# Optimization experiments

Hardware: AMD Instinct MI355X
Metric: run time of the kernel (lower is better)

Reference implementation:

```python
import jax, jax.numpy as jnp
import numpy as np

N = 200000
F_IN = 165
H = 128
E = 3200000


def gcn_conv(x, edge_index, W, b):
    # x: [N, Fin], edge_index: [2, E], W: [Fin, Fout], b: [Fout]
    n = x.shape[0]
    h = x @ W  # linear transform first (PyG GCNConv)
    # add self loops
    loops = jnp.arange(n, dtype=edge_index.dtype)
    src = jnp.concatenate([edge_index[0], loops])
    dst = jnp.concatenate([edge_index[1], loops])
    # symmetric normalization: deg computed on dst (in-degree incl. self loops)
    deg = jax.ops.segment_sum(jnp.ones_like(dst, dtype=h.dtype), dst, num_segments=n)
    dinv = jnp.where(deg > 0, jax.lax.rsqrt(deg), 0.0)
    norm = dinv[src] * dinv[dst]  # [E+N]
    msgs = h[src] * norm[:, None]  # gather + scale
    out = jax.ops.segment_sum(msgs, dst, num_segments=n)  # scatter-add
    return out + b


def setup_inputs() -> dict:
    key = jax.random.key(0)
    k = jax.random.split(key, 8)
    x = jax.random.normal(k[0], (N, F_IN), dtype=jnp.float32)
    edge_index = jax.random.randint(k[1], (2, E), 0, N, dtype=jnp.int64)
    s1 = 1.0 / np.sqrt(F_IN)
    s2 = 1.0 / np.sqrt(H)
    W1 = jax.random.uniform(k[2], (F_IN, H), jnp.float32, -s1, s1)
    b1 = jnp.zeros((H,), jnp.float32)
    W2 = jax.random.uniform(k[3], (H, H), jnp.float32, -s2, s2)
    b2 = jnp.zeros((H,), jnp.float32)
    Wl = jax.random.uniform(k[4], (H, 2), jnp.float32, -s2, s2)
    bl = jax.random.uniform(k[5], (2,), jnp.float32, -s2, s2)
    return {"x": x, "edge_index": edge_index, "W1": W1, "b1": b1,
            "W2": W2, "b2": b2, "Wl": Wl, "bl": bl}


def reference(x, edge_index, W1, b1, W2, b2, Wl, bl):
    h = gcn_conv(x, edge_index, W1, b1)
    h = jax.nn.relu(h)
    # dropout p=0.3 is identity in eval mode
    h = gcn_conv(h, edge_index, W2, b2)
    h = jax.nn.relu(h)
    return h @ Wl + bl  # [N, 2]
```

## Files before the change

### kernel.cpp

```cpp
#include <hip/hip_runtime.h>
#include <hip/hip_bf16.h>

#define FIN 165
#define HID 128
#define NPB 256
#define MAXNB 784
#define CAP 4608
#define EPB 4096

typedef __attribute__((ext_vector_type(8))) short short8;
typedef __attribute__((ext_vector_type(4))) float float4v;

__device__ inline unsigned bf16rne(float v) {
    unsigned u = __float_as_uint(v);
    return (u + 0x7fffu + ((u >> 16) & 1u)) >> 16;
}

__device__ inline void bf16split(float v, short& h, short& l) {
    unsigned u = __float_as_uint(v);
    unsigned r = u + 0x7fffu + ((u >> 16) & 1u);
    h = (short)(r >> 16);
    float hf = __uint_as_float(((unsigned)(unsigned short)h) << 16);
    float lf = v - hf;
    unsigned u2 = __float_as_uint(lf);
    unsigned r2 = u2 + 0x7fffu + ((u2 >> 16) & 1u);
    l = (short)(r2 >> 16);
}

__global__ __launch_bounds__(256) void bucket_scatter(const int* __restrict__ src,
                                                      const int* __restrict__ dst,
                                                      int* __restrict__ gcur,
                                                      int2* __restrict__ bucketed,
                                                      int E, int n, int NB) {
    __shared__ int hist[MAXNB];
    __shared__ int base[MAXNB];
    __shared__ int lcur[MAXNB];
    int tid = threadIdx.x;
    long e0 = (long)blockIdx.x * EPB;
    for (int b = tid; b < NB; b += 256) { hist[b] = 0; lcur[b] = 0; }
    __syncthreads();
#pragma unroll
    for (int i = 0; i < EPB / 256; ++i) {
        long e = e0 + i * 256 + tid;
        if (e < E) {
            int d = dst[e], s = src[e];
            if ((unsigned)d < (unsigned)n && (unsigned)s < (unsigned)n)
                atomicAdd(&hist[d >> 8], 1);
        }
    }
    __syncthreads();
    for (int b = tid; b < NB; b += 256) {
        int h = hist[b];
        base[b] = h ? atomicAdd(&gcur[b * 16], h) : 0;
    }
    __syncthreads();
#pragma unroll
    for (int i = 0; i < EPB / 256; ++i) {
        long e = e0 + i * 256 + tid;
        if (e < E) {
            int d = dst[e], s = src[e];
            if ((unsigned)d < (unsigned)n && (unsigned)s < (unsigned)n) {
                int bk = d >> 8;
                int idx = base[bk] + atomicAdd(&lcur[bk], 1);
                if ((unsigned)idx < (unsigned)CAP)
                    bucketed[(size_t)bk * CAP + idx] = make_int2(s, d);
            }
        }
    }
}

__global__ __launch_bounds__(256) void bucket_scan(const int* __restrict__ gcur,
                                                   int* __restrict__ bb, int NB,
                                                   int* __restrict__ rowptr, int n) {
    __shared__ int sm[MAXNB];
    for (int b = threadIdx.x; b < NB; b += 256) sm[b] = gcur[b * 16];
    __syncthreads();
    if (threadIdx.x == 0) {
        int run = 0;
        for (int b = 0; b < NB; ++b) { int c = sm[b]; sm[b] = run; run += c; }
        bb[NB] = run;
        rowptr[n] = run;
    }
    __syncthreads();
    for (int b = threadIdx.x; b < NB; b += 256) bb[b] = sm[b];
}

__global__ __launch_bounds__(256) void build_csr(const int2* __restrict__ bucketed,
                                                 const int* __restrict__ bb,
                                                 float* __restrict__ dinv,
                                                 int* __restrict__ rowptr,
                                                 int* __restrict__ col, int n) {
    __shared__ int deg[NPB];
    __shared__ int scn[NPB];
    __shared__ int cur[NPB];
    int b = blockIdx.x, tid = threadIdx.x;
    int nb0 = b * NPB;
    int ebase = bb[b], cnt = bb[b + 1] - bb[b];
    deg[tid] = 0;
    __syncthreads();
    const int2* ep = bucketed + (size_t)b * CAP;
    for (int i = tid; i < cnt; i += 256) {
        int2 e = ep[i];
        atomicAdd(&deg[e.y - nb0], 1);
    }
    __syncthreads();
    int d = deg[tid];
    scn[tid] = d;
    __syncthreads();
    for (int off = 1; off < 256; off <<= 1) {
        int v = (tid >= off) ? scn[tid - off] : 0;
        __syncthreads();
        scn[tid] += v;
        __syncthreads();
    }
    int excl = scn[tid] - d;
    int node = nb0 + tid;
    if (node < n) {
        dinv[node] = rsqrtf((float)(d + 1));
        rowptr[node] = ebase + excl;
    }
    cur[tid] = excl;
    __syncthreads();
    for (int i = tid; i < cnt; i += 256) {
        int2 e = ep[i];
        int p = atomicAdd(&cur[e.y - nb0], 1);
        col[ebase + p] = e.x;
    }
}

__global__ __launch_bounds__(256) void wswz(const float* __restrict__ W,
                                            short8* __restrict__ out, int K, int k32) {
    int idx = blockIdx.x * 256 + threadIdx.x;
    int tot = k32 * 8 * 64;
    if (idx >= tot) return;
    int lane = idx & 63;
    int ct = (idx >> 6) & 7;
    int ks = idx >> 9;
    int col = ct * 16 + (lane & 15);
    int kb = ks * 32 + (lane >> 4) * 8;
    short8 hi, lo;
#pragma unroll
    for (int j = 0; j < 8; ++j) {
        int k = kb + j;
        float v = (k < K) ? W[k * HID + col] : 0.f;
        short h, l;
        bf16split(v, h, l);
        hi[j] = h; lo[j] = l;
    }
    out[idx] = hi;
    out[tot + idx] = lo;
}

__global__ __launch_bounds__(256) void gemm_mfma(const float* __restrict__ X,
                                                 const short8* __restrict__ Wsw,
                                                 const float* __restrict__ dinv,
                                                 unsigned* __restrict__ H2,
                                                 int n, int K, int kfull, int k32) {
    int wave = threadIdx.x >> 6, lane = threadIdx.x & 63;
    int r0 = blockIdx.x * 64 + wave * 16;
    int m = lane & 15, kph = lane >> 4;
    int row = r0 + m;
    const float* xrow = X + (size_t)row * K + kph * 8;
    const short8* Whi = Wsw;
    const short8* Wlo = Wsw + (size_t)k32 * 8 * 64;

    float4v acc[8];
#pragma unroll
    for (int ct = 0; ct < 8; ++ct) acc[ct] = (float4v){0.f, 0.f, 0.f, 0.f};

    for (int ks = 0; ks < kfull; ++ks) {
        float xv[8];
#pragma unroll
        for (int j = 0; j < 8; ++j) xv[j] = xrow[ks * 32 + j];
        short8 ah, al;
#pragma unroll
        for (int j = 0; j < 8; ++j) {
            short h, l; bf16split(xv[j], h, l);
            ah[j] = h; al[j] = l;
        }
#pragma unroll
        for (int ct = 0; ct < 8; ++ct) {
            short8 bh = Whi[(ks * 8 + ct) * 64 + lane];
            short8 bl = Wlo[(ks * 8 + ct) * 64 + lane];
            acc[ct] = __builtin_amdgcn_mfma_f32_16x16x32_bf16(ah, bh, acc[ct], 0, 0, 0);
            acc[ct] = __builtin_amdgcn_mfma_f32_16x16x32_bf16(al, bh, acc[ct], 0, 0, 0);
            acc[ct] = __builtin_amdgcn_mfma_f32_16x16x32_bf16(ah, bl, acc[ct], 0, 0, 0);
        }
    }
    if (kfull < k32) {
        int ks = kfull;
        int kb = ks * 32 + kph * 8;
        float xv[8];
#pragma unroll
        for (int j = 0; j < 8; ++j) xv[j] = (kb + j < K) ? xrow[ks * 32 + j] : 0.f;
        short8 ah, al;
#pragma unroll
        for (int j = 0; j < 8; ++j) {
            short h, l; bf16split(xv[j], h, l);
            ah[j] = h; al[j] = l;
        }
#pragma unroll
        for (int ct = 0; ct < 8; ++ct) {
            short8 bh = Whi[(ks * 8 + ct) * 64 + lane];
            short8 bl = Wlo[(ks * 8 + ct) * 64 + lane];
            acc[ct] = __builtin_amdgcn_mfma_f32_16x16x32_bf16(ah, bh, acc[ct], 0, 0, 0);
            acc[ct] = __builtin_amdgcn_mfma_f32_16x16x32_bf16(al, bh, acc[ct], 0, 0, 0);
            acc[ct] = __builtin_amdgcn_mfma_f32_16x16x32_bf16(ah, bl, acc[ct], 0, 0, 0);
        }
    }
    int ccol = lane & 15, crow = (lane >> 4) * 4;
    bool evenl = (ccol & 1) == 0;
#pragma unroll
    for (int r = 0; r < 4; ++r) {
        int gr = r0 + crow + r;
        float s = dinv[gr];
#pragma unroll
        for (int ct = 0; ct < 8; ++ct) {
            float v = acc[ct][r] * s;
            float p = __shfl_xor(v, 1);
            if (evenl) {
                unsigned u = bf16rne(v) | (bf16rne(p) << 16);
                H2[(size_t)gr * 64 + ct * 8 + (ccol >> 1)] = u;
            }
        }
    }
}

__device__ inline void bf2_unpack(unsigned u, float& f0, float& f1) {
    f0 = __uint_as_float(u << 16);
    f1 = __uint_as_float(u & 0xffff0000u);
}

__global__ __launch_bounds__(256) void agg_relu(const unsigned* __restrict__ HS2,
                                                const int* __restrict__ rowptr,
                                                const int* __restrict__ col,
                                                const float* __restrict__ dinv,
                                                const float* __restrict__ bias,
                                                float* __restrict__ Y, int n) {
    int node = blockIdx.x * 4 + (threadIdx.x >> 6);
    int lane = threadIdx.x & 63;
    if (node >= n) return;
    int start = rowptr[node], end = rowptr[node + 1];
    float2 acc;
    {
        float f0, f1;
        bf2_unpack(HS2[(size_t)node * 64 + lane], f0, f1);
        acc.x = f0; acc.y = f1;
    }
    for (int j0 = start; j0 < end; j0 += 64) {
        int cnt = min(64, end - j0);
        int cv = (j0 + lane < end) ? col[j0 + lane] : 0;
        int t = 0;
        for (; t + 8 <= cnt; t += 8) {
            unsigned uv[8];
#pragma unroll
            for (int q = 0; q < 8; ++q) {
                int c = __shfl(cv, t + q);
                uv[q] = HS2[(size_t)c * 64 + lane];
            }
#pragma unroll
            for (int q = 0; q < 8; ++q) {
                float f0, f1; bf2_unpack(uv[q], f0, f1);
                acc.x += f0; acc.y += f1;
            }
        }
        for (; t < cnt; ++t) {
            int c = __shfl(cv, t);
            float f0, f1; bf2_unpack(HS2[(size_t)c * 64 + lane], f0, f1);
            acc.x += f0; acc.y += f1;
        }
    }
    float s = dinv[node];
    float2 b = *(const float2*)&bias[2 * lane];
    float2 o;
    o.x = fmaxf(acc.x * s + b.x, 0.f);
    o.y = fmaxf(acc.y * s + b.y, 0.f);
    *(float2*)&Y[(long)node * HID + 2 * lane] = o;
}

__global__ __launch_bounds__(256) void agg_relu_head(const unsigned* __restrict__ HS2,
                                                     const int* __restrict__ rowptr,
                                                     const int* __restrict__ col,
                                                     const float* __restrict__ dinv,
                                                     const float* __restrict__ bias,
                                                     const float* __restrict__ Wl,
                                                     const float* __restrict__ bl,
                                                     float* __restrict__ out, int n) {
    int node = blockIdx.x * 4 + (threadIdx.x >> 6);
    int lane = threadIdx.x & 63;
    if (node >= n) return;
    int start = rowptr[node], end = rowptr[node + 1];
    float2 acc;
    {
        float f0, f1;
        bf2_unpack(HS2[(size_t)node * 64 + lane], f0, f1);
        acc.x = f0; acc.y = f1;
    }
    for (int j0 = start; j0 < end; j0 += 64) {
        int cnt = min(64, end - j0);
        int cv = (j0 + lane < end) ? col[j0 + lane] : 0;
        int t = 0;
        for (; t + 8 <= cnt; t += 8) {
            unsigned uv[8];
#pragma unroll
            for (int q = 0; q < 8; ++q) {
                int c = __shfl(cv, t + q);
                uv[q] = HS2[(size_t)c * 64 + lane];
            }
#pragma unroll
            for (int q = 0; q < 8; ++q) {
                float f0, f1; bf2_unpack(uv[q], f0, f1);
                acc.x += f0; acc.y += f1;
            }
        }
        for (; t < cnt; ++t) {
            int c = __shfl(cv, t);
            float f0, f1; bf2_unpack(HS2[(size_t)c * 64 + lane], f0, f1);
            acc.x += f0; acc.y += f1;
        }
    }
    float s = dinv[node];
    float2 b = *(const float2*)&bias[2 * lane];
    float vx = fmaxf(acc.x * s + b.x, 0.f);
    float vy = fmaxf(acc.y * s + b.y, 0.f);
    float4 wl = *(const float4*)&Wl[4 * lane];
    float a0 = vx * wl.x + vy * wl.z;
    float a1 = vx * wl.y + vy * wl.w;
#pragma unroll
    for (int off = 32; off > 0; off >>= 1) {
        a0 += __shfl_xor(a0, off);
        a1 += __shfl_xor(a1, off);
    }
    if (lane == 0) {
        out[node * 2 + 0] = a0 + bl[0];
        out[node * 2 + 1] = a1 + bl[1];
    }
}

extern "C" void kernel_launch(void* const* d_in, const int* in_sizes, int n_in,
                              void* d_out, int out_size, void* d_ws, size_t ws_size,
                              hipStream_t stream) {
    const float* x  = (const float*)d_in[0];
    const int*   ei = (const int*)d_in[1];
    const float* W1 = (const float*)d_in[2];
    const float* b1 = (const float*)d_in[3];
    const float* W2 = (const float*)d_in[4];
    const float* b2 = (const float*)d_in[5];
    const float* Wl = (const float*)d_in[6];
    const float* bl = (const float*)d_in[7];
    float* out = (float*)d_out;

    int n = in_sizes[0] / FIN;
    int E = in_sizes[1] / 2;
    int NB = (n + NPB - 1) / NPB;
    const int* srcp = ei;
    const int* dstp = ei + E;

    char* w = (char*)d_ws;
    auto alloc = [&](size_t bytes) {
        char* p = w;
        w += (bytes + 255) & ~(size_t)255;
        return (void*)p;
    };
    int*      gcur    = (int*)     alloc((size_t)NB * 16 * 4);
    int*      bb      = (int*)     alloc(((size_t)NB + 1) * 4);
    int*      rowptr  = (int*)     alloc(((size_t)n + 1) * 4);
    float*    dinv    = (float*)   alloc((size_t)n * 4);
    int*      colv    = (int*)     alloc((size_t)E * 4);
    unsigned* hbuf    = (unsigned*)alloc((size_t)n * 64 * 4);
    float*    ybuf    = (float*)   alloc((size_t)n * HID * 4);
    const int K32_1 = (FIN + 31) / 32;
    const int K32_2 = HID / 32;
    short8*   w1sw    = (short8*)  alloc((size_t)2 * K32_1 * 8 * 64 * 16);
    short8*   w2sw    = (short8*)  alloc((size_t)2 * K32_2 * 8 * 64 * 16);
    int2*     bucketed = (int2*)ybuf;

    hipMemsetAsync(gcur, 0, (size_t)NB * 16 * 4, stream);

    wswz<<<(K32_1 * 8 * 64 + 255) / 256, 256, 0, stream>>>(W1, w1sw, FIN, K32_1);
    wswz<<<(K32_2 * 8 * 64 + 255) / 256, 256, 0, stream>>>(W2, w2sw, HID, K32_2);

    bucket_scatter<<<(E + EPB - 1) / EPB, 256, 0, stream>>>(srcp, dstp, gcur,
                                                            bucketed, E, n, NB);
    bucket_scan<<<1, 256, 0, stream>>>(gcur, bb, NB, rowptr, n);
    build_csr<<<NB, 256, 0, stream>>>(bucketed, bb, dinv, rowptr, colv, n);

    gemm_mfma<<<n / 64, 256, 0, stream>>>(x, w1sw, dinv, hbuf, n, FIN, FIN / 32, K32_1);
    agg_relu<<<(n + 3) / 4, 256, 0, stream>>>(hbuf, rowptr, colv, dinv, b1, ybuf, n);

    gemm_mfma<<<n / 64, 256, 0, stream>>>(ybuf, w2sw, dinv, hbuf, n, HID, HID / 32, K32_2);

    agg_relu_head<<<(n + 3) / 4, 256, 0, stream>>>(hbuf, rowptr, colv, dinv, b2,
                                                   Wl, bl, out, n);
}
```

Baseline: 724.9 us.

## Persistent-wave aggregation with triple-buffered gathers spanning node boundaries

Replaces the one-wave-per-node aggregation with a persistent grid of 4096 blocks, where each wave walks a contiguous range of nodes. Neighbor gathers are issued in chunks of eight into three rotating register buffers, so loads for the next chunk, including chunks belonging to the next node, are in flight while the current chunk is summed. The self-loop is handled as the index-minus-one slot, and tail slots are masked. This aims to hide gather latency and cut per-node launch and tail overhead. In exchange it adds register pressure, per-element bounds clamping, and load imbalance across waves when degrees vary.

```diff
diff --git a/kernel.cpp b/kernel.cpp
--- a/kernel.cpp
+++ b/kernel.cpp
@@ -7,6 +7,7 @@
 #define MAXNB 784
 #define CAP 4608
 #define EPB 4096
+#define AGG_BLOCKS 4096
 
 typedef __attribute__((ext_vector_type(8))) short short8;
 typedef __attribute__((ext_vector_type(4))) float float4v;
@@ -231,51 +232,85 @@
     f1 = __uint_as_float(u & 0xffff0000u);
 }
 
+struct Buf8 { unsigned v[8]; };
+struct RSt { int j, e, nd; bool last; };
+
+#define AGG_ISSUE(BUF, ST)                                                         \
+    {                                                                              \
+        ST.j = jI; ST.e = eI; ST.nd = nI; ST.last = (jI + 8 >= eI);                \
+        _Pragma("unroll")                                                          \
+        for (int q = 0; q < 8; ++q) {                                              \
+            int jq = jI + q;                                                       \
+            int jcl = min(max(jq, sI), eI - 1);                                    \
+            int cl = col[jcl];                      \
+            int c = (jq >= sI && jq < eI) ? cl : nI;                               \
+            BUF.v[q] = HS2[(size_t)c * 64 + lane];                                 \
+        }                                                                          \
+        jI += 8;                                                                   \
+        if (jI >= eI) {                                                            \
+            if (nI + 1 >= n1) doneI = true;                                        \
+            else { nI += 1; sI = eI; eI = rowptr[nI + 1]; jI = sI - 1; }           \
+        }                                                                          \
+    }
+
+#define AGG_CONSUME(BUF, ST, FINALIZE)                                             \
+    {                                                                              \
+        _Pragma("unroll")                                                          \
+        for (int q = 0; q < 8; ++q) {                                              \
+            unsigned u = (ST.j + q < ST.e) ? BUF.v[q] : 0u;                        \
+            float f0, f1; bf2_unpack(u, f0, f1);                                   \
+            accx += f0; accy += f1;                                                \
+        }                                                                          \
+        if (ST.last) { FINALIZE(ST.nd); accx = 0.f; accy = 0.f; }                  \
+    }
+
 __global__ __launch_bounds__(256) void agg_relu(const unsigned* __restrict__ HS2,
                                                 const int* __restrict__ rowptr,
                                                 const int* __restrict__ col,
                                                 const float* __restrict__ dinv,
                                                 const float* __restrict__ bias,
                                                 float* __restrict__ Y, int n) {
-    int node = blockIdx.x * 4 + (threadIdx.x >> 6);
     int lane = threadIdx.x & 63;
-    if (node >= n) return;
-    int start = rowptr[node], end = rowptr[node + 1];
-    float2 acc;
-    {
-        float f0, f1;
-        bf2_unpack(HS2[(size_t)node * 64 + lane], f0, f1);
-        acc.x = f0; acc.y = f1;
-    }
-    for (int j0 = start; j0 < end; j0 += 64) {
-        int cnt = min(64, end - j0);
-        int cv = (j0 + lane < end) ? col[j0 + lane] : 0;
-        int t = 0;
-        for (; t + 8 <= cnt; t += 8) {
-            unsigned uv[8];
-#pragma unroll
-            for (int q = 0; q < 8; ++q) {
-                int c = __shfl(cv, t + q);
-                uv[q] = HS2[(size_t)c * 64 + lane];
-            }
-#pragma unroll
-            for (int q = 0; q < 8; ++q) {
-                float f0, f1; bf2_unpack(uv[q], f0, f1);
-                acc.x += f0; acc.y += f1;
-            }
-        }
-        for (; t < cnt; ++t) {
-            int c = __shfl(cv, t);
-            float f0, f1; bf2_unpack(HS2[(size_t)c * 64 + lane], f0, f1);
-            acc.x += f0; acc.y += f1;
-        }
-    }
-    float s = dinv[node];
+    int wid = __builtin_amdgcn_readfirstlane(blockIdx.x * 4 + (threadIdx.x >> 6));
+    int waves = gridDim.x * 4;
+    int C = (n + waves - 1) / waves;
+    int n0 = wid * C;
+    if (n0 >= n) return;
+    int n1 = min(n0 + C, n);
+
+    int nI = n0;
+    int sI = __builtin_amdgcn_readfirstlane(rowptr[n0]);
+    int eI = __builtin_amdgcn_readfirstlane(rowptr[n0 + 1]);
+    int jI = sI - 1;
+    bool doneI = false;
+
+    float accx = 0.f, accy = 0.f;
     float2 b = *(const float2*)&bias[2 * lane];
-    float2 o;
-    o.x = fmaxf(acc.x * s + b.x, 0.f);
-    o.y = fmaxf(acc.y * s + b.y, 0.f);
-    *(float2*)&Y[(long)node * HID + 2 * lane] = o;
+    Buf8 A, B_, Cb;
+    RSt rA, rB, rC;
+
+#define FIN_RELU(ND)                                                               \
+    {                                                                              \
+        float s = dinv[ND];                                                        \
+        float2 o;                                                                  \
+        o.x = fmaxf(accx * s + b.x, 0.f);                                          \
+        o.y = fmaxf(accy * s + b.y, 0.f);                                          \
+        *(float2*)&Y[(long)(ND) * HID + 2 * lane] = o;                             \
+    }
+
+    AGG_ISSUE(A, rA);
+    for (;;) {
+        if (doneI) { AGG_CONSUME(A, rA, FIN_RELU); break; }
+        AGG_ISSUE(B_, rB);
+        AGG_CONSUME(A, rA, FIN_RELU);
+        if (doneI) { AGG_CONSUME(B_, rB, FIN_RELU); break; }
+        AGG_ISSUE(Cb, rC);
+        AGG_CONSUME(B_, rB, FIN_RELU);
+        if (doneI) { AGG_CONSUME(Cb, rC, FIN_RELU); break; }
+        AGG_ISSUE(A, rA);
+        AGG_CONSUME(Cb, rC, FIN_RELU);
+    }
+#undef FIN_RELU
 }
 
 __global__ __launch_bounds__(256) void agg_relu_head(const unsigned* __restrict__ HS2,
@@ -286,55 +321,58 @@
                                                      const float* __restrict__ Wl,
                                                      const float* __restrict__ bl,
                                                      float* __restrict__ out, int n) {
-    int node = blockIdx.x * 4 + (threadIdx.x >> 6);
     int lane = threadIdx.x & 63;
-    if (node >= n) return;
-    int start = rowptr[node], end = rowptr[node + 1];
-    float2 acc;
-    {
-        float f0, f1;
-        bf2_unpack(HS2[(size_t)node * 64 + lane], f0, f1);
-        acc.x = f0; acc.y = f1;
-    }
-    for (int j0 = start; j0 < end; j0 += 64) {
-        int cnt = min(64, end - j0);
-        int cv = (j0 + lane < end) ? col[j0 + lane] : 0;
-        int t = 0;
-        for (; t + 8 <= cnt; t += 8) {
-            unsigned uv[8];
-#pragma unroll
-            for (int q = 0; q < 8; ++q) {
-                int c = __shfl(cv, t + q);
-                uv[q] = HS2[(size_t)c * 64 + lane];
-            }
-#pragma unroll
-            for (int q = 0; q < 8; ++q) {
-                float f0, f1; bf2_unpack(uv[q], f0, f1);
-                acc.x += f0; acc.y += f1;
-            }
-        }
-        for (; t < cnt; ++t) {
-            int c = __shfl(cv, t);
-            float f0, f1; bf2_unpack(HS2[(size_t)c * 64 + lane], f0, f1);
-            acc.x += f0; acc.y += f1;
-        }
-    }
-    float s = dinv[node];
+    int wid = __builtin_amdgcn_readfirstlane(blockIdx.x * 4 + (threadIdx.x >> 6));
+    int waves = gridDim.x * 4;
+    int C = (n + waves - 1) / waves;
+    int n0 = wid * C;
+    if (n0 >= n) return;
+    int n1 = min(n0 + C, n);
+
+    int nI = n0;
+    int sI = __builtin_amdgcn_readfirstlane(rowptr[n0]);
+    int eI = __builtin_amdgcn_readfirstlane(rowptr[n0 + 1]);
+    int jI = sI - 1;
+    bool doneI = false;
+
+    float accx = 0.f, accy = 0.f;
     float2 b = *(const float2*)&bias[2 * lane];
-    float vx = fmaxf(acc.x * s + b.x, 0.f);
-    float vy = fmaxf(acc.y * s + b.y, 0.f);
     float4 wl = *(const float4*)&Wl[4 * lane];
-    float a0 = vx * wl.x + vy * wl.z;
-    float a1 = vx * wl.y + vy * wl.w;
-#pragma unroll
-    for (int off = 32; off > 0; off >>= 1) {
-        a0 += __shfl_xor(a0, off);
-        a1 += __shfl_xor(a1, off);
-    }
-    if (lane == 0) {
-        out[node * 2 + 0] = a0 + bl[0];
-        out[node * 2 + 1] = a1 + bl[1];
-    }
+    float bl0 = bl[0], bl1 = bl[1];
+    Buf8 A, B_, Cb;
+    RSt rA, rB, rC;
+
+#define FIN_HEAD(ND)                                                               \
+    {                                                                              \
+        float s = dinv[ND];                                                        \
+        float vx = fmaxf(accx * s + b.x, 0.f);                                     \
+        float vy = fmaxf(accy * s + b.y, 0.f);                                     \
+        float a0 = vx * wl.x + vy * wl.z;                                          \
+        float a1 = vx * wl.y + vy * wl.w;                                          \
+        _Pragma("unroll")                                                          \
+        for (int off = 32; off > 0; off >>= 1) {                                   \
+            a0 += __shfl_xor(a0, off);                                             \
+            a1 += __shfl_xor(a1, off);                                             \
+        }                                                                          \
+        if (lane == 0) {                                                           \
+            out[(long)(ND) * 2 + 0] = a0 + bl0;                                    \
+            out[(long)(ND) * 2 + 1] = a1 + bl1;                                    \
+        }                                                                          \
+    }
+
+    AGG_ISSUE(A, rA);
+    for (;;) {
+        if (doneI) { AGG_CONSUME(A, rA, FIN_HEAD); break; }
+        AGG_ISSUE(B_, rB);
+        AGG_CONSUME(A, rA, FIN_HEAD);
+        if (doneI) { AGG_CONSUME(B_, rB, FIN_HEAD); break; }
+        AGG_ISSUE(Cb, rC);
+        AGG_CONSUME(B_, rB, FIN_HEAD);
+        if (doneI) { AGG_CONSUME(Cb, rC, FIN_HEAD); break; }
+        AGG_ISSUE(A, rA);
+        AGG_CONSUME(Cb, rC, FIN_HEAD);
+    }
+#undef FIN_HEAD
 }
 
 extern "C" void kernel_launch(void* const* d_in, const int* in_sizes, int n_in,
@@ -386,10 +424,10 @@
     build_csr<<<NB, 256, 0, stream>>>(bucketed, bb, dinv, rowptr, colv, n);
 
     gemm_mfma<<<n / 64, 256, 0, stream>>>(x, w1sw, dinv, hbuf, n, FIN, FIN / 32, K32_1);
-    agg_relu<<<(n + 3) / 4, 256, 0, stream>>>(hbuf, rowptr, colv, dinv, b1, ybuf, n);
+    agg_relu<<<AGG_BLOCKS, 256, 0, stream>>>(hbuf, rowptr, colv, dinv, b1, ybuf, n);
 
     gemm_mfma<<<n / 64, 256, 0, stream>>>(ybuf, w2sw, dinv, hbuf, n, HID, HID / 32, K32_2);
 
-    agg_relu_head<<<(n + 3) / 4, 256, 0, stream>>>(hbuf, rowptr, colv, dinv, b2,
-                                                   Wl, bl, out, n);
-}
+    agg_relu_head<<<AGG_BLOCKS, 256, 0, stream>>>(hbuf, rowptr, colv, dinv, b2,
+                                                  Wl, bl, out, n);
+}
```

Result: slower. 786.5 us (+8.5%).
